# Kernel tuning notes

Measured on AMD Instinct MI355X. Metric: run time of the kernel, lower is better.

The kernel has to match this reference:

```python
import jax, jax.numpy as jnp
import numpy as np

B, T, D, H = 4, 2048, 512, 8
DH = D // H  # 64
EPS = 1e-5


def setup_inputs() -> dict:
    key = jax.random.key(0)
    ks = jax.random.split(key, 12)
    s = lambda k, shp, fan: jax.random.normal(k, shp, jnp.float32) * (fan ** -0.5)
    return {
        "x": jax.random.normal(ks[0], (B, T, D), jnp.float32),
        "ln1_g": jnp.ones((D,), jnp.float32),
        "ln1_b": jnp.zeros((D,), jnp.float32),
        "Wq": s(ks[1], (H, D, DH), D),  # per-head bias-free projections
        "Wk": s(ks[2], (H, D, DH), D),
        "Wv": s(ks[3], (H, D, DH), D),
        "Wproj": s(ks[4], (D, D), D),
        "bproj": jnp.zeros((D,), jnp.float32),
        "W1": s(ks[5], (D, 4 * D), D),
        "b1": jnp.zeros((4 * D,), jnp.float32),
        "W2": s(ks[6], (4 * D, D), 4 * D),
        "b2": jnp.zeros((D,), jnp.float32),
    }


def _layernorm(x, g, b):
    m = jnp.mean(x, axis=-1, keepdims=True)
    v = jnp.var(x, axis=-1, keepdims=True)
    return (x - m) * jax.lax.rsqrt(v + EPS) * g + b


def reference(x, ln1_g, ln1_b, Wq, Wk, Wv, Wproj, bproj, W1, b1, W2, b2):
    b, t, c = x.shape
    scale = c ** -0.5  # source scales by input channel dim, not head_size
    causal = jnp.tril(jnp.ones((t, t), bool))  # [T,T]

    # --- attention sublayer (pre-norm with ln1) ---
    h = _layernorm(x, ln1_g, ln1_b)
    q = jnp.einsum('btd,hde->bhte', h, Wq)
    k = jnp.einsum('btd,hde->bhte', h, Wk)
    v = jnp.einsum('btd,hde->bhte', h, Wv)
    scores = jnp.einsum('bhte,bhse->bhts', q, k) * scale  # [B,H,T,T]
    scores = jnp.where(causal, scores, -jnp.inf)
    att = jax.nn.softmax(scores, axis=-1)  # dropout = identity at inference
    o = jnp.einsum('bhts,bhse->bthe', att, v).reshape(b, t, c)  # concat heads
    sa = o @ Wproj + bproj
    x = x + sa

    # --- FFN sublayer (source reuses ln1, faithful) ---
    h2 = _layernorm(x, ln1_g, ln1_b)
    ff = jax.nn.relu(h2 @ W1 + b1) @ W2 + b2
    return x + ff
```

## Files before the change

### kernel.cpp

```cpp
#include <hip/hip_runtime.h>
#include <math.h>

#define B_ 4
#define T_ 2048
#define D_ 512
#define H_ 8
#define DH_ 64
#define BT_ 8192
#define FF_ 2048
#define EPS_ 1e-5f
#define SCALE_ 0.04419417382415922f
#define SC2_ 0.06375861151f
#define NEGINF_ -1e30f

typedef short b16x8 __attribute__((ext_vector_type(8)));
typedef short b16x4 __attribute__((ext_vector_type(4)));
typedef float f32x4 __attribute__((ext_vector_type(4)));

#define MFMA16(a, b, c) __builtin_amdgcn_mfma_f32_16x16x32_bf16(a, b, c, 0, 0, 0)
#define MFMA16K16(a, b, c) __builtin_amdgcn_mfma_f32_16x16x16bf16_1k(a, b, c, 0, 0, 0)

#define GLL16(gp, lp) \
    __builtin_amdgcn_global_load_lds((const __attribute__((address_space(1))) void*)(gp), \
                                     (__attribute__((address_space(3))) void*)(lp), 16, 0, 0)

#if __has_builtin(__builtin_amdgcn_exp2f)
#define EXP2F(x) __builtin_amdgcn_exp2f(x)
#else
#define EXP2F(x) exp2f(x)
#endif

static __device__ inline short f2bf(float f) {
    unsigned int u = __builtin_bit_cast(unsigned int, f);
    unsigned int r = (u + 0x7fffu + ((u >> 16) & 1u)) >> 16;
    return (short)r;
}
static __device__ inline short f2bf_trunc(float f) {
    return (short)(__builtin_bit_cast(unsigned int, f) >> 16);
}

__global__ __launch_bounds__(64) void ln_kernel(const float* __restrict__ X,
        const float* __restrict__ G, const float* __restrict__ Bb,
        short* __restrict__ Y)
{
    int row = blockIdx.x;
    int t = threadIdx.x;
    const float* xr = X + (size_t)row * D_;
    float4 v0 = *(const float4*)(xr + t * 4);
    float4 v1 = *(const float4*)(xr + 256 + t * 4);
    float sum = v0.x + v0.y + v0.z + v0.w + v1.x + v1.y + v1.z + v1.w;
    float ssq = v0.x*v0.x + v0.y*v0.y + v0.z*v0.z + v0.w*v0.w
              + v1.x*v1.x + v1.y*v1.y + v1.z*v1.z + v1.w*v1.w;
    #pragma unroll
    for (int off = 32; off > 0; off >>= 1) {
        sum += __shfl_down(sum, off);
        ssq += __shfl_down(ssq, off);
    }
    sum = __shfl(sum, 0);
    ssq = __shfl(ssq, 0);
    float mean = sum * (1.0f / D_);
    float var  = ssq * (1.0f / D_) - mean * mean;
    float rstd = rsqrtf(var + EPS_);

    float4 g0 = *(const float4*)(G + t * 4);
    float4 g1 = *(const float4*)(G + 256 + t * 4);
    float4 b0 = *(const float4*)(Bb + t * 4);
    float4 b1 = *(const float4*)(Bb + 256 + t * 4);
    short4 o0, o1;
    o0.x = f2bf((v0.x - mean) * rstd * g0.x + b0.x);
    o0.y = f2bf((v0.y - mean) * rstd * g0.y + b0.y);
    o0.z = f2bf((v0.z - mean) * rstd * g0.z + b0.z);
    o0.w = f2bf((v0.w - mean) * rstd * g0.w + b0.w);
    o1.x = f2bf((v1.x - mean) * rstd * g1.x + b1.x);
    o1.y = f2bf((v1.y - mean) * rstd * g1.y + b1.y);
    o1.z = f2bf((v1.z - mean) * rstd * g1.z + b1.z);
    o1.w = f2bf((v1.w - mean) * rstd * g1.w + b1.w);
    short* yr = Y + (size_t)row * D_;
    *(short4*)(yr + t * 4)       = o0;
    *(short4*)(yr + 256 + t * 4) = o1;
}

__global__ __launch_bounds__(256) void prep_kernel(
        const float* __restrict__ Wq, const float* __restrict__ Wk,
        const float* __restrict__ Wv, const float* __restrict__ Wp,
        const float* __restrict__ W1, const float* __restrict__ W2,
        short* __restrict__ wqkv, short* __restrict__ wpt,
        short* __restrict__ w1t, short* __restrict__ w2t)
{
    __shared__ float tile[32][33];
    int idx = blockIdx.x;
    const float* src; short* dst; int R, C, tx0, ty0;
    if (idx < 768) {
        int w = idx >> 8, rem = idx & 255;
        int hh = rem >> 5, t = rem & 31;
        const float* base = (w == 0) ? Wq : ((w == 1) ? Wk : Wv);
        src = base + hh * (D_ * DH_);
        dst = wqkv + w * (512 * 512) + hh * (DH_ * D_);
        R = 512; C = 64; tx0 = (t & 1) * 32; ty0 = (t >> 1) * 32;
    } else if (idx < 1024) {
        int t = idx - 768;
        src = Wp; dst = wpt; R = 512; C = 512;
        tx0 = (t & 15) * 32; ty0 = (t >> 4) * 32;
    } else if (idx < 2048) {
        int t = idx - 1024;
        src = W1; dst = w1t; R = 512; C = 2048;
        tx0 = (t & 63) * 32; ty0 = (t >> 6) * 32;
    } else {
        int t = idx - 2048;
        src = W2; dst = w2t; R = 2048; C = 512;
        tx0 = (t & 15) * 32; ty0 = (t >> 4) * 32;
    }
    int tx = threadIdx.x, ty = threadIdx.y;
    #pragma unroll
    for (int i = 0; i < 32; i += 8)
        tile[ty + i][tx] = src[(size_t)(ty0 + ty + i) * C + tx0 + tx];
    __syncthreads();
    #pragma unroll
    for (int i = 0; i < 32; i += 8)
        dst[(size_t)(tx0 + ty + i) * R + ty0 + tx] = f2bf(tile[tx][ty + i]);
}

__global__ __launch_bounds__(256) void mm_kernel(const short* __restrict__ A,
        const short* __restrict__ Bt, void* __restrict__ C,
        const float* __restrict__ bias, const float* __restrict__ resid,
        int M, int N, int K, int relu, int out_bf16)
{
    __shared__ short As[128 * 64];
    __shared__ short Bs[128 * 64];
    const int tid = threadIdx.x;
    const int wave = tid >> 6, lane = tid & 63;
    const int quad = lane >> 4, l15 = lane & 15;
    const int m0 = blockIdx.x * 128, n0 = blockIdx.y * 128;
    const int mw = (wave & 1) * 64, nw = (wave >> 1) * 64;

    f32x4 acc[4][4];
    #pragma unroll
    for (int i = 0; i < 4; ++i)
        #pragma unroll
        for (int j = 0; j < 4; ++j)
            acc[i][j] = (f32x4){0.f, 0.f, 0.f, 0.f};

    for (int k0 = 0; k0 < K; k0 += 64) {
        __syncthreads();
        #pragma unroll
        for (int r = 0; r < 4; ++r) {
            int c = r * 256 + tid;
            int row = c >> 3, seg = (c & 7) ^ (row & 7);
            GLL16(A + (size_t)(m0 + row) * K + k0 + seg * 8,
                  As + (size_t)(r * 256 + wave * 64) * 8);
            GLL16(Bt + (size_t)(n0 + row) * K + k0 + seg * 8,
                  Bs + (size_t)(r * 256 + wave * 64) * 8);
        }
        __syncthreads();
        b16x8 af[4][2], bf[4][2];
        #pragma unroll
        for (int i = 0; i < 4; ++i)
            #pragma unroll
            for (int kb = 0; kb < 2; ++kb) {
                int row = mw + i * 16 + l15;
                af[i][kb] = *(const b16x8*)(As + row * 64 + (((kb * 4 + quad) ^ (row & 7)) * 8));
            }
        #pragma unroll
        for (int j = 0; j < 4; ++j)
            #pragma unroll
            for (int kb = 0; kb < 2; ++kb) {
                int row = nw + j * 16 + l15;
                bf[j][kb] = *(const b16x8*)(Bs + row * 64 + (((kb * 4 + quad) ^ (row & 7)) * 8));
            }
        #pragma unroll
        for (int kb = 0; kb < 2; ++kb)
            #pragma unroll
            for (int i = 0; i < 4; ++i)
                #pragma unroll
                for (int j = 0; j < 4; ++j)
                    acc[i][j] = MFMA16(af[i][kb], bf[j][kb], acc[i][j]);
    }

    #pragma unroll
    for (int i = 0; i < 4; ++i) {
        #pragma unroll
        for (int r = 0; r < 4; ++r) {
            size_t row = (size_t)(m0 + mw + i * 16 + quad * 4 + r);
            #pragma unroll
            for (int j = 0; j < 4; ++j) {
                int col = n0 + nw + j * 16 + l15;
                float v = acc[i][j][r];
                if (bias)  v += bias[col];
                if (resid) v += resid[row * N + col];
                if (relu)  v = fmaxf(v, 0.0f);
                if (out_bf16) ((short*)C)[row * N + col] = f2bf(v);
                else          ((float*)C)[row * N + col] = v;
            }
        }
    }
}

__global__ __launch_bounds__(256) void mm64_kernel(const short* __restrict__ A,
        const short* __restrict__ Bt, void* __restrict__ C,
        const float* __restrict__ bias, const float* __restrict__ resid,
        int M, int N, int K, int relu, int out_bf16)
{
    __shared__ short As[128 * 64];
    __shared__ short Bs[64 * 64];
    const int tid = threadIdx.x;
    const int wave = tid >> 6, lane = tid & 63;
    const int quad = lane >> 4, l15 = lane & 15;
    const int m0 = blockIdx.x * 128, n0 = blockIdx.y * 64;
    const int mw = (wave & 1) * 64, nw = (wave >> 1) * 32;

    f32x4 acc[4][2];
    #pragma unroll
    for (int i = 0; i < 4; ++i)
        #pragma unroll
        for (int j = 0; j < 2; ++j)
            acc[i][j] = (f32x4){0.f, 0.f, 0.f, 0.f};

    for (int k0 = 0; k0 < K; k0 += 64) {
        __syncthreads();
        #pragma unroll
        for (int r = 0; r < 4; ++r) {
            int c = r * 256 + tid;
            int row = c >> 3, seg = (c & 7) ^ (row & 7);
            GLL16(A + (size_t)(m0 + row) * K + k0 + seg * 8,
                  As + (size_t)(r * 256 + wave * 64) * 8);
        }
        #pragma unroll
        for (int r = 0; r < 2; ++r) {
            int c = r * 256 + tid;
            int row = c >> 3, seg = (c & 7) ^ (row & 7);
            GLL16(Bt + (size_t)(n0 + row) * K + k0 + seg * 8,
                  Bs + (size_t)(r * 256 + wave * 64) * 8);
        }
        __syncthreads();
        b16x8 af[4][2], bf[2][2];
        #pragma unroll
        for (int i = 0; i < 4; ++i)
            #pragma unroll
            for (int kb = 0; kb < 2; ++kb) {
                int row = mw + i * 16 + l15;
                af[i][kb] = *(const b16x8*)(As + row * 64 + (((kb * 4 + quad) ^ (row & 7)) * 8));
            }
        #pragma unroll
        for (int j = 0; j < 2; ++j)
            #pragma unroll
            for (int kb = 0; kb < 2; ++kb) {
                int row = nw + j * 16 + l15;
                bf[j][kb] = *(const b16x8*)(Bs + row * 64 + (((kb * 4 + quad) ^ (row & 7)) * 8));
            }
        #pragma unroll
        for (int kb = 0; kb < 2; ++kb)
            #pragma unroll
            for (int i = 0; i < 4; ++i)
                #pragma unroll
                for (int j = 0; j < 2; ++j)
                    acc[i][j] = MFMA16(af[i][kb], bf[j][kb], acc[i][j]);
    }

    #pragma unroll
    for (int i = 0; i < 4; ++i) {
        #pragma unroll
        for (int r = 0; r < 4; ++r) {
            size_t row = (size_t)(m0 + mw + i * 16 + quad * 4 + r);
            #pragma unroll
            for (int j = 0; j < 2; ++j) {
                int col = n0 + nw + j * 16 + l15;
                float v = acc[i][j][r];
                if (bias)  v += bias[col];
                if (resid) v += resid[row * N + col];
                if (relu)  v = fmaxf(v, 0.0f);
                if (out_bf16) ((short*)C)[row * N + col] = f2bf(v);
                else          ((float*)C)[row * N + col] = v;
            }
        }
    }
}

__global__ __launch_bounds__(256) void mm6464_kernel(const short* __restrict__ A,
        const short* __restrict__ Bt, void* __restrict__ C,
        const float* __restrict__ bias, const float* __restrict__ resid,
        int M, int N, int K, int relu, int out_bf16)
{
    __shared__ short As[64 * 64];
    __shared__ short Bs[64 * 64];
    const int tid = threadIdx.x;
    const int wave = tid >> 6, lane = tid & 63;
    const int quad = lane >> 4, l15 = lane & 15;
    const int m0 = blockIdx.x * 64, n0 = blockIdx.y * 64;
    const int nw = wave * 16;

    f32x4 acc[4];
    #pragma unroll
    for (int i = 0; i < 4; ++i) acc[i] = (f32x4){0.f, 0.f, 0.f, 0.f};

    for (int k0 = 0; k0 < K; k0 += 64) {
        __syncthreads();
        #pragma unroll
        for (int r = 0; r < 2; ++r) {
            int c = r * 256 + tid;
            int row = c >> 3, seg = (c & 7) ^ (row & 7);
            GLL16(A + (size_t)(m0 + row) * K + k0 + seg * 8,
                  As + (size_t)(r * 256 + wave * 64) * 8);
            GLL16(Bt + (size_t)(n0 + row) * K + k0 + seg * 8,
                  Bs + (size_t)(r * 256 + wave * 64) * 8);
        }
        __syncthreads();
        b16x8 af[4][2], bf[2];
        #pragma unroll
        for (int i = 0; i < 4; ++i)
            #pragma unroll
            for (int kb = 0; kb < 2; ++kb) {
                int row = i * 16 + l15;
                af[i][kb] = *(const b16x8*)(As + row * 64 + (((kb * 4 + quad) ^ (row & 7)) * 8));
            }
        #pragma unroll
        for (int kb = 0; kb < 2; ++kb) {
            int row = nw + l15;
            bf[kb] = *(const b16x8*)(Bs + row * 64 + (((kb * 4 + quad) ^ (row & 7)) * 8));
        }
        #pragma unroll
        for (int kb = 0; kb < 2; ++kb)
            #pragma unroll
            for (int i = 0; i < 4; ++i)
                acc[i] = MFMA16(af[i][kb], bf[kb], acc[i]);
    }

    #pragma unroll
    for (int i = 0; i < 4; ++i) {
        #pragma unroll
        for (int r = 0; r < 4; ++r) {
            size_t row = (size_t)(m0 + i * 16 + quad * 4 + r);
            int col = n0 + nw + l15;
            float v = acc[i][r];
            if (bias)  v += bias[col];
            if (resid) v += resid[row * N + col];
            if (relu)  v = fmaxf(v, 0.0f);
            if (out_bf16) ((short*)C)[row * N + col] = f2bf(v);
            else          ((float*)C)[row * N + col] = v;
        }
    }
}

__global__ __launch_bounds__(256) void attn_kernel(const short* __restrict__ qkv,
        short* __restrict__ Ob)
{
    __shared__ short Qs[64 * 64];
    __shared__ short Ks[64 * 64];
    __shared__ short Vt[64 * 72];
    __shared__ short Osh[64 * 72];

    const int tid = threadIdx.x;
    const int wave = tid >> 6, lane = tid & 63;
    const int quad = lane >> 4, l15 = lane & 15;
    const int bh = blockIdx.x;
    const int qi = 31 - (int)blockIdx.y;
    const int b = bh >> 3, h = bh & 7;
    const size_t tok0 = (size_t)b * T_;
    const int qrow_rel = wave * 16 + l15;

    #pragma unroll
    for (int r = 0; r < 2; ++r) {
        int c = r * 256 + tid;
        int tk = c >> 3;
        int seg = (c & 7) ^ (tk & 7);
        GLL16(qkv + (tok0 + qi * 64 + tk) * 1536 + h * 64 + seg * 8,
              Qs + (size_t)(r * 256 + wave * 64) * 8);
    }

    float mrow = NEGINF_, lrow = 0.0f;
    f32x4 ot[4];
    #pragma unroll
    for (int dt = 0; dt < 4; ++dt) ot[dt] = (f32x4){0.f, 0.f, 0.f, 0.f};

    b16x8 qf[2];

    for (int kj = 0; kj <= qi; ++kj) {
        __syncthreads();
        #pragma unroll
        for (int r = 0; r < 2; ++r) {
            int c = r * 256 + tid;
            int tk = c >> 3;
            int seg = (c & 7) ^ (tk & 7);
            GLL16(qkv + (tok0 + kj * 64 + tk) * 1536 + 512 + h * 64 + seg * 8,
                  Ks + (size_t)(r * 256 + wave * 64) * 8);
        }
        {
            int s = tid >> 5, tp = tid & 31;
            const short* g0 = qkv + (tok0 + kj * 64 + tp * 2) * 1536 + 1024 + h * 64 + s * 8;
            b16x8 v0 = *(const b16x8*)g0;
            b16x8 v1 = *(const b16x8*)(g0 + 1536);
            int* vo = (int*)Vt;
            #pragma unroll
            for (int e = 0; e < 8; ++e) {
                unsigned int pk = (unsigned int)(unsigned short)v0[e]
                                | ((unsigned int)(unsigned short)v1[e] << 16);
                vo[(s * 8 + e) * 36 + tp] = pk;
            }
        }
        __syncthreads();

        if (kj == 0) {
            #pragma unroll
            for (int kb = 0; kb < 2; ++kb) {
                int row = wave * 16 + l15;
                qf[kb] = *(const b16x8*)(Qs + row * 64 + (((kb * 4 + quad) ^ (row & 7)) * 8));
            }
        }

        f32x4 st[4];
        #pragma unroll
        for (int mt = 0; mt < 4; ++mt) st[mt] = (f32x4){0.f, 0.f, 0.f, 0.f};
        #pragma unroll
        for (int mt = 0; mt < 4; ++mt) {
            int trow = mt * 16 + l15;
            #pragma unroll
            for (int kb = 0; kb < 2; ++kb) {
                b16x8 kf = *(const b16x8*)(Ks + trow * 64 + (((kb * 4 + quad) ^ (trow & 7)) * 8));
                st[mt] = MFMA16(kf, qf[kb], st[mt]);
            }
        }

        const bool diag = (kj == qi);
        float mx = NEGINF_;
        #pragma unroll
        for (int mt = 0; mt < 4; ++mt)
            #pragma unroll
            for (int r = 0; r < 4; ++r) {
                if (diag && (mt * 16 + quad * 4 + r) > qrow_rel) st[mt][r] = NEGINF_;
                mx = fmaxf(mx, st[mt][r]);
            }
        mx = fmaxf(mx, __shfl_xor(mx, 16));
        mx = fmaxf(mx, __shfl_xor(mx, 32));
        float mn = fmaxf(mrow, mx);
        float alpha = EXP2F((mrow - mn) * SC2_);
        float mnsc = mn * SC2_;
        mrow = mn;
        float rs = 0.0f;
        b16x4 pf[4];
        #pragma unroll
        for (int mt = 0; mt < 4; ++mt)
            #pragma unroll
            for (int r = 0; r < 4; ++r) {
                float e = EXP2F(fmaf(st[mt][r], SC2_, -mnsc));
                rs += e;
                pf[mt][r] = f2bf_trunc(e);
            }
        rs += __shfl_xor(rs, 16);
        rs += __shfl_xor(rs, 32);
        lrow = lrow * alpha + rs;
        #pragma unroll
        for (int dt = 0; dt < 4; ++dt) {
            ot[dt][0] *= alpha; ot[dt][1] *= alpha;
            ot[dt][2] *= alpha; ot[dt][3] *= alpha;
        }
        #pragma unroll
        for (int dt = 0; dt < 4; ++dt) {
            const short* vrow = Vt + (dt * 16 + l15) * 72;
            #pragma unroll
            for (int kt = 0; kt < 4; ++kt) {
                b16x4 vf = *(const b16x4*)(vrow + kt * 16 + quad * 4);
                ot[dt] = MFMA16K16(vf, pf[kt], ot[dt]);
            }
        }
    }

    float inv = 1.0f / lrow;
    #pragma unroll
    for (int dt = 0; dt < 4; ++dt) {
        b16x4 o4;
        o4[0] = f2bf(ot[dt][0] * inv);
        o4[1] = f2bf(ot[dt][1] * inv);
        o4[2] = f2bf(ot[dt][2] * inv);
        o4[3] = f2bf(ot[dt][3] * inv);
        *(b16x4*)(Osh + (size_t)qrow_rel * 72 + dt * 16 + quad * 4) = o4;
    }
    {
        int row = tid >> 2, ch = tid & 3;
        b16x8 lo = *(const b16x8*)(Osh + (size_t)row * 72 + ch * 16);
        b16x8 hi = *(const b16x8*)(Osh + (size_t)row * 72 + ch * 16 + 8);
        short* dst = Ob + (tok0 + (size_t)qi * 64 + row) * 512 + h * 64 + ch * 16;
        *(b16x8*)dst = lo;
        *(b16x8*)(dst + 8) = hi;
    }
}

extern "C" void kernel_launch(void* const* d_in, const int* in_sizes, int n_in,
                              void* d_out, int out_size, void* d_ws, size_t ws_size,
                              hipStream_t stream) {
    (void)in_sizes; (void)n_in; (void)out_size; (void)ws_size;
    const float* x     = (const float*)d_in[0];
    const float* ln_g  = (const float*)d_in[1];
    const float* ln_b  = (const float*)d_in[2];
    const float* Wq    = (const float*)d_in[3];
    const float* Wk    = (const float*)d_in[4];
    const float* Wv    = (const float*)d_in[5];
    const float* Wproj = (const float*)d_in[6];
    const float* bproj = (const float*)d_in[7];
    const float* W1    = (const float*)d_in[8];
    const float* b1    = (const float*)d_in[9];
    const float* W2    = (const float*)d_in[10];
    const float* b2    = (const float*)d_in[11];
    float* out = (float*)d_out;

    char* W = (char*)d_ws;
    short* hbuf  = (short*)(W + 0);
    short* qkvb  = (short*)(W + ((size_t)8  << 20));
    short* attno = (short*)(W + ((size_t)32 << 20));
    float* x1    = (float*)(W + ((size_t)40 << 20));
    short* ff1   = (short*)(W + ((size_t)56 << 20));
    short* wqkv  = (short*)(W + ((size_t)88 << 20));
    short* wpt   = (short*)(W + ((size_t)90 << 20));
    short* w1t   = (short*)(W + ((size_t)91 << 20));
    short* w2t   = (short*)(W + ((size_t)93 << 20));

    prep_kernel<<<dim3(3072), dim3(32, 8), 0, stream>>>(
        Wq, Wk, Wv, Wproj, W1, W2, wqkv, wpt, w1t, w2t);
    ln_kernel<<<dim3(BT_), dim3(64), 0, stream>>>(x, ln_g, ln_b, hbuf);
    mm_kernel<<<dim3(64, 12), dim3(256), 0, stream>>>(hbuf, wqkv, qkvb,
        nullptr, nullptr, BT_, 1536, D_, 0, 1);
    attn_kernel<<<dim3(32, 32), dim3(256), 0, stream>>>(qkvb, attno);
    mm6464_kernel<<<dim3(128, 8), dim3(256), 0, stream>>>(attno, wpt, x1,
        bproj, x, BT_, D_, D_, 0, 0);
    ln_kernel<<<dim3(BT_), dim3(64), 0, stream>>>(x1, ln_g, ln_b, hbuf);
    mm_kernel<<<dim3(64, 16), dim3(256), 0, stream>>>(hbuf, w1t, ff1,
        b1, nullptr, BT_, FF_, D_, 1, 1);
    mm64_kernel<<<dim3(64, 8), dim3(256), 0, stream>>>(ff1, w2t, out,
        b2, x1, BT_, D_, FF_, 0, 0);
}
```

Baseline: 298.7 us.

## Double-buffer GEMM LDS tiles with K=32 stages and XOR-swizzle V transpose

All three GEMM kernels move from single-buffered 64-wide K tiles with two barriers per step to double-buffered 32-wide K tiles. The next tile's global-to-LDS load is issued before computing on the current one, so there is one barrier per step and memory latency can overlap with MFMA work. The attention kernel's transposed V tile drops its 72-element padding for an XOR swizzle, saving LDS while still avoiding bank conflicts. The trade-off is twice as many barriers and loop iterations per K, less MFMA work per sync, and a new load being in flight while other waves read the buffer being refilled.

```diff
diff --git a/kernel.cpp b/kernel.cpp
--- a/kernel.cpp
+++ b/kernel.cpp
@@ -125,14 +125,26 @@
         const float* __restrict__ bias, const float* __restrict__ resid,
         int M, int N, int K, int relu, int out_bf16)
 {
-    __shared__ short As[128 * 64];
-    __shared__ short Bs[128 * 64];
+    __shared__ short As[2][128 * 32];
+    __shared__ short Bs[2][128 * 32];
     const int tid = threadIdx.x;
     const int wave = tid >> 6, lane = tid & 63;
     const int quad = lane >> 4, l15 = lane & 15;
     const int m0 = blockIdx.x * 128, n0 = blockIdx.y * 128;
     const int mw = (wave & 1) * 64, nw = (wave >> 1) * 64;
 
+#define STAGE_MM(bufi, kk) \
+    { \
+        for (int r = 0; r < 2; ++r) { \
+            int c = r * 256 + tid; \
+            int row = c >> 2, seg = (c & 3) ^ (row & 3); \
+            GLL16(A + (size_t)(m0 + row) * K + (kk) + seg * 8, \
+                  As[bufi] + (size_t)(r * 256 + wave * 64) * 8); \
+            GLL16(Bt + (size_t)(n0 + row) * K + (kk) + seg * 8, \
+                  Bs[bufi] + (size_t)(r * 256 + wave * 64) * 8); \
+        } \
+    }
+
     f32x4 acc[4][4];
     #pragma unroll
     for (int i = 0; i < 4; ++i)
@@ -140,41 +152,30 @@
         for (int j = 0; j < 4; ++j)
             acc[i][j] = (f32x4){0.f, 0.f, 0.f, 0.f};
 
-    for (int k0 = 0; k0 < K; k0 += 64) {
+    STAGE_MM(0, 0);
+    int buf = 0;
+    for (int k0 = 0; k0 < K; k0 += 32) {
         __syncthreads();
-        #pragma unroll
-        for (int r = 0; r < 4; ++r) {
-            int c = r * 256 + tid;
-            int row = c >> 3, seg = (c & 7) ^ (row & 7);
-            GLL16(A + (size_t)(m0 + row) * K + k0 + seg * 8,
-                  As + (size_t)(r * 256 + wave * 64) * 8);
-            GLL16(Bt + (size_t)(n0 + row) * K + k0 + seg * 8,
-                  Bs + (size_t)(r * 256 + wave * 64) * 8);
-        }
-        __syncthreads();
-        b16x8 af[4][2], bf[4][2];
+        if (k0 + 32 < K) STAGE_MM(buf ^ 1, k0 + 32);
+        b16x8 af[4], bf[4];
+        #pragma unroll
+        for (int i = 0; i < 4; ++i) {
+            int row = mw + i * 16 + l15;
+            af[i] = *(const b16x8*)(As[buf] + row * 32 + ((quad ^ (row & 3)) * 8));
+        }
+        #pragma unroll
+        for (int j = 0; j < 4; ++j) {
+            int row = nw + j * 16 + l15;
+            bf[j] = *(const b16x8*)(Bs[buf] + row * 32 + ((quad ^ (row & 3)) * 8));
+        }
         #pragma unroll
         for (int i = 0; i < 4; ++i)
             #pragma unroll
-            for (int kb = 0; kb < 2; ++kb) {
-                int row = mw + i * 16 + l15;
-                af[i][kb] = *(const b16x8*)(As + row * 64 + (((kb * 4 + quad) ^ (row & 7)) * 8));
-            }
-        #pragma unroll
-        for (int j = 0; j < 4; ++j)
-            #pragma unroll
-            for (int kb = 0; kb < 2; ++kb) {
-                int row = nw + j * 16 + l15;
-                bf[j][kb] = *(const b16x8*)(Bs + row * 64 + (((kb * 4 + quad) ^ (row & 7)) * 8));
-            }
-        #pragma unroll
-        for (int kb = 0; kb < 2; ++kb)
-            #pragma unroll
-            for (int i = 0; i < 4; ++i)
-                #pragma unroll
-                for (int j = 0; j < 4; ++j)
-                    acc[i][j] = MFMA16(af[i][kb], bf[j][kb], acc[i][j]);
-    }
+            for (int j = 0; j < 4; ++j)
+                acc[i][j] = MFMA16(af[i], bf[j], acc[i][j]);
+        buf ^= 1;
+    }
+#undef STAGE_MM
 
     #pragma unroll
     for (int i = 0; i < 4; ++i) {
@@ -200,14 +201,29 @@
         const float* __restrict__ bias, const float* __restrict__ resid,
         int M, int N, int K, int relu, int out_bf16)
 {
-    __shared__ short As[128 * 64];
-    __shared__ short Bs[64 * 64];
+    __shared__ short As[2][128 * 32];
+    __shared__ short Bs[2][64 * 32];
     const int tid = threadIdx.x;
     const int wave = tid >> 6, lane = tid & 63;
     const int quad = lane >> 4, l15 = lane & 15;
     const int m0 = blockIdx.x * 128, n0 = blockIdx.y * 64;
     const int mw = (wave & 1) * 64, nw = (wave >> 1) * 32;
 
+#define STAGE_M64(bufi, kk) \
+    { \
+        for (int r = 0; r < 2; ++r) { \
+            int c = r * 256 + tid; \
+            int row = c >> 2, seg = (c & 3) ^ (row & 3); \
+            GLL16(A + (size_t)(m0 + row) * K + (kk) + seg * 8, \
+                  As[bufi] + (size_t)(r * 256 + wave * 64) * 8); \
+        } \
+        { \
+            int row = tid >> 2, seg = (tid & 3) ^ (row & 3); \
+            GLL16(Bt + (size_t)(n0 + row) * K + (kk) + seg * 8, \
+                  Bs[bufi] + (size_t)(wave * 64) * 8); \
+        } \
+    }
+
     f32x4 acc[4][2];
     #pragma unroll
     for (int i = 0; i < 4; ++i)
@@ -215,46 +231,30 @@
         for (int j = 0; j < 2; ++j)
             acc[i][j] = (f32x4){0.f, 0.f, 0.f, 0.f};
 
-    for (int k0 = 0; k0 < K; k0 += 64) {
+    STAGE_M64(0, 0);
+    int buf = 0;
+    for (int k0 = 0; k0 < K; k0 += 32) {
         __syncthreads();
-        #pragma unroll
-        for (int r = 0; r < 4; ++r) {
-            int c = r * 256 + tid;
-            int row = c >> 3, seg = (c & 7) ^ (row & 7);
-            GLL16(A + (size_t)(m0 + row) * K + k0 + seg * 8,
-                  As + (size_t)(r * 256 + wave * 64) * 8);
-        }
-        #pragma unroll
-        for (int r = 0; r < 2; ++r) {
-            int c = r * 256 + tid;
-            int row = c >> 3, seg = (c & 7) ^ (row & 7);
-            GLL16(Bt + (size_t)(n0 + row) * K + k0 + seg * 8,
-                  Bs + (size_t)(r * 256 + wave * 64) * 8);
-        }
-        __syncthreads();
-        b16x8 af[4][2], bf[2][2];
+        if (k0 + 32 < K) STAGE_M64(buf ^ 1, k0 + 32);
+        b16x8 af[4], bf[2];
+        #pragma unroll
+        for (int i = 0; i < 4; ++i) {
+            int row = mw + i * 16 + l15;
+            af[i] = *(const b16x8*)(As[buf] + row * 32 + ((quad ^ (row & 3)) * 8));
+        }
+        #pragma unroll
+        for (int j = 0; j < 2; ++j) {
+            int row = nw + j * 16 + l15;
+            bf[j] = *(const b16x8*)(Bs[buf] + row * 32 + ((quad ^ (row & 3)) * 8));
+        }
         #pragma unroll
         for (int i = 0; i < 4; ++i)
             #pragma unroll
-            for (int kb = 0; kb < 2; ++kb) {
-                int row = mw + i * 16 + l15;
-                af[i][kb] = *(const b16x8*)(As + row * 64 + (((kb * 4 + quad) ^ (row & 7)) * 8));
-            }
-        #pragma unroll
-        for (int j = 0; j < 2; ++j)
-            #pragma unroll
-            for (int kb = 0; kb < 2; ++kb) {
-                int row = nw + j * 16 + l15;
-                bf[j][kb] = *(const b16x8*)(Bs + row * 64 + (((kb * 4 + quad) ^ (row & 7)) * 8));
-            }
-        #pragma unroll
-        for (int kb = 0; kb < 2; ++kb)
-            #pragma unroll
-            for (int i = 0; i < 4; ++i)
-                #pragma unroll
-                for (int j = 0; j < 2; ++j)
-                    acc[i][j] = MFMA16(af[i][kb], bf[j][kb], acc[i][j]);
-    }
+            for (int j = 0; j < 2; ++j)
+                acc[i][j] = MFMA16(af[i], bf[j], acc[i][j]);
+        buf ^= 1;
+    }
+#undef STAGE_M64
 
     #pragma unroll
     for (int i = 0; i < 4; ++i) {
@@ -280,49 +280,48 @@
         const float* __restrict__ bias, const float* __restrict__ resid,
         int M, int N, int K, int relu, int out_bf16)
 {
-    __shared__ short As[64 * 64];
-    __shared__ short Bs[64 * 64];
+    __shared__ short As[2][64 * 32];
+    __shared__ short Bs[2][64 * 32];
     const int tid = threadIdx.x;
     const int wave = tid >> 6, lane = tid & 63;
     const int quad = lane >> 4, l15 = lane & 15;
     const int m0 = blockIdx.x * 64, n0 = blockIdx.y * 64;
     const int nw = wave * 16;
 
+#define STAGE_M66(bufi, kk) \
+    { \
+        int row = tid >> 2, seg = (tid & 3) ^ (row & 3); \
+        GLL16(A + (size_t)(m0 + row) * K + (kk) + seg * 8, \
+              As[bufi] + (size_t)(wave * 64) * 8); \
+        GLL16(Bt + (size_t)(n0 + row) * K + (kk) + seg * 8, \
+              Bs[bufi] + (size_t)(wave * 64) * 8); \
+    }
+
     f32x4 acc[4];
     #pragma unroll
     for (int i = 0; i < 4; ++i) acc[i] = (f32x4){0.f, 0.f, 0.f, 0.f};
 
-    for (int k0 = 0; k0 < K; k0 += 64) {
+    STAGE_M66(0, 0);
+    int buf = 0;
+    for (int k0 = 0; k0 < K; k0 += 32) {
         __syncthreads();
-        #pragma unroll
-        for (int r = 0; r < 2; ++r) {
-            int c = r * 256 + tid;
-            int row = c >> 3, seg = (c & 7) ^ (row & 7);
-            GLL16(A + (size_t)(m0 + row) * K + k0 + seg * 8,
-                  As + (size_t)(r * 256 + wave * 64) * 8);
-            GLL16(Bt + (size_t)(n0 + row) * K + k0 + seg * 8,
-                  Bs + (size_t)(r * 256 + wave * 64) * 8);
-        }
-        __syncthreads();
-        b16x8 af[4][2], bf[2];
+        if (k0 + 32 < K) STAGE_M66(buf ^ 1, k0 + 32);
+        b16x8 af[4], bf;
+        #pragma unroll
+        for (int i = 0; i < 4; ++i) {
+            int row = i * 16 + l15;
+            af[i] = *(const b16x8*)(As[buf] + row * 32 + ((quad ^ (row & 3)) * 8));
+        }
+        {
+            int row = nw + l15;
+            bf = *(const b16x8*)(Bs[buf] + row * 32 + ((quad ^ (row & 3)) * 8));
+        }
         #pragma unroll
         for (int i = 0; i < 4; ++i)
-            #pragma unroll
-            for (int kb = 0; kb < 2; ++kb) {
-                int row = i * 16 + l15;
-                af[i][kb] = *(const b16x8*)(As + row * 64 + (((kb * 4 + quad) ^ (row & 7)) * 8));
-            }
-        #pragma unroll
-        for (int kb = 0; kb < 2; ++kb) {
-            int row = nw + l15;
-            bf[kb] = *(const b16x8*)(Bs + row * 64 + (((kb * 4 + quad) ^ (row & 7)) * 8));
-        }
-        #pragma unroll
-        for (int kb = 0; kb < 2; ++kb)
-            #pragma unroll
-            for (int i = 0; i < 4; ++i)
-                acc[i] = MFMA16(af[i][kb], bf[kb], acc[i]);
-    }
+            acc[i] = MFMA16(af[i], bf, acc[i]);
+        buf ^= 1;
+    }
+#undef STAGE_M66
 
     #pragma unroll
     for (int i = 0; i < 4; ++i) {
@@ -345,7 +344,7 @@
 {
     __shared__ short Qs[64 * 64];
     __shared__ short Ks[64 * 64];
-    __shared__ short Vt[64 * 72];
+    __shared__ short Vt[64 * 64];
     __shared__ short Osh[64 * 72];
 
     const int tid = threadIdx.x;
@@ -389,11 +388,13 @@
             b16x8 v0 = *(const b16x8*)g0;
             b16x8 v1 = *(const b16x8*)(g0 + 1536);
             int* vo = (int*)Vt;
+            int gg = tp >> 1, half = tp & 1;
             #pragma unroll
             for (int e = 0; e < 8; ++e) {
+                int row = s * 8 + e;
                 unsigned int pk = (unsigned int)(unsigned short)v0[e]
                                 | ((unsigned int)(unsigned short)v1[e] << 16);
-                vo[(s * 8 + e) * 36 + tp] = pk;
+                vo[row * 32 + ((gg ^ (row & 15)) << 1) + half] = pk;
             }
         }
         __syncthreads();
@@ -454,10 +455,10 @@
         }
         #pragma unroll
         for (int dt = 0; dt < 4; ++dt) {
-            const short* vrow = Vt + (dt * 16 + l15) * 72;
+            const short* vrow = Vt + (dt * 16 + l15) * 64;
             #pragma unroll
             for (int kt = 0; kt < 4; ++kt) {
-                b16x4 vf = *(const b16x4*)(vrow + kt * 16 + quad * 4);
+                b16x4 vf = *(const b16x4*)(vrow + (((kt * 4 + quad) ^ l15) << 2));
                 ot[dt] = MFMA16K16(vf, pf[kt], ot[dt]);
             }
         }
```

Result: no change. 294.5 us (-1.4%).
